# Optimization experiments

Measured on AMD Instinct MI355X. Metric: run time of the kernel, lower is better.

## Reference

```python
import jax, jax.numpy as jnp
import numpy as np

EPS = 1e-5
B, C, N_A, N_B, P, M = 128, 32, 12, 12, 8192, 2


def _bn(x, gamma, beta, mean, var):
    # x: (B, C, P); per-channel inference batch norm
    scale = gamma * jax.lax.rsqrt(var + EPS)
    return x * scale[None, :, None] + (beta - mean * scale)[None, :, None]


def setup_inputs() -> dict:
    key = jax.random.key(0)
    ks = jax.random.split(key, 12)
    return {
        "feat_a": jax.random.normal(ks[0], (B, C, N_A), jnp.float32),
        "feat_b": jax.random.normal(ks[1], (B, C, N_B), jnp.float32),
        "assign_a": jax.random.randint(ks[2], (P, M), 0, N_A, jnp.int32),
        "assign_b": jax.random.randint(ks[3], (P, M), 0, N_B, jnp.int32),
        "bn1_gamma": jax.random.uniform(ks[4], (C,), jnp.float32, 0.5, 1.5),
        "bn1_beta": jax.random.normal(ks[5], (C,), jnp.float32) * 0.1,
        "bn1_mean": jax.random.normal(ks[6], (C,), jnp.float32) * 0.1,
        "bn1_var": jax.random.uniform(ks[7], (C,), jnp.float32, 0.5, 1.5),
        "conv_w": jax.random.normal(ks[8], (C, C), jnp.float32) / np.sqrt(C),
        "bn2_gamma": jax.random.uniform(ks[9], (C,), jnp.float32, 0.5, 1.5),
        "bn2_beta": jax.random.normal(ks[10], (C,), jnp.float32) * 0.1,
        "bn2_mean": jax.random.normal(ks[11], (C,), jnp.float32) * 0.1,
        "bn2_var": jnp.ones((C,), jnp.float32),
    }


def reference(feat_a, feat_b, assign_a, assign_b,
              bn1_gamma, bn1_beta, bn1_mean, bn1_var,
              conv_w, bn2_gamma, bn2_beta, bn2_mean, bn2_var):
    # Gather product features via permutation indices: (B, C, P, M)
    ga = feat_a[:, :, assign_a].max(axis=-1)  # max over constituents -> (B, C, P)
    gb = feat_b[:, :, assign_b].max(axis=-1)
    agg = jnp.maximum(ga, gb)                 # 'max' aggregation across products
    x = _bn(agg, bn1_gamma, bn1_beta, bn1_mean, bn1_var)
    x = jnp.einsum('oc,bcp->bop', conv_w, x)  # 1x1 Conv1d, no bias
    x = _bn(x, bn2_gamma, bn2_beta, bn2_mean, bn2_var)
    return jax.nn.relu(x)
```

## Files before the change

kernel.cpp:

```cpp
#include <hip/hip_runtime.h>


#define EPS 1e-5f
constexpr int B   = 128;
constexpr int C   = 32;
constexpr int NA  = 12;
constexpr int PP  = 8192;
constexpr int PT  = 256;
constexpr int FS  = 36;
constexpr int XS  = 40;
constexpr int W2S = 36;

typedef short bfv8  __attribute__((ext_vector_type(8)));
typedef float f32x4 __attribute__((ext_vector_type(4)));

__device__ __forceinline__ ushort f2bf(float f) {
    uint u = __float_as_uint(f);
    u += 0x7fffu + ((u >> 16) & 1u);
    return (ushort)(u >> 16);
}
__device__ __forceinline__ float bf2f(ushort h) {
    return __uint_as_float(((uint)h) << 16);
}
__device__ __forceinline__ uint pk(ushort lo, ushort hi) {
    return (uint)lo | ((uint)hi << 16);
}

__global__ __launch_bounds__(256) void main_kernel(
    const float* __restrict__ feat_a, const float* __restrict__ feat_b,
    const int*   __restrict__ assign_a, const int* __restrict__ assign_b,
    const float* __restrict__ conv_w,
    const float* __restrict__ g1, const float* __restrict__ b1,
    const float* __restrict__ m1, const float* __restrict__ v1,
    const float* __restrict__ g2, const float* __restrict__ b2,
    const float* __restrict__ m2, const float* __restrict__ v2,
    float* __restrict__ out)
{
    __shared__ float s1[C], t1[C], s2v[C], bsh[C];
    __shared__ __align__(16) float  w2[C * W2S];
    __shared__ __align__(16) float  fa[NA * FS];
    __shared__ __align__(16) float  fb[NA * FS];
    __shared__ __align__(16) ushort xh[PT * XS];

    const int tid  = threadIdx.x;
    const int lane = tid & 63;
    const int b    = blockIdx.x >> 5;
    const int p0   = (blockIdx.x & 31) * PT;
    const int q    = lane >> 4;
    const int n    = lane & 15;

    if (tid < C) {
        float s = g1[tid] * rsqrtf(v1[tid] + EPS);
        s1[tid]  = s;
        t1[tid]  = b1[tid] - m1[tid] * s;
        s2v[tid] = g2[tid] * rsqrtf(v2[tid] + EPS);
    }
    for (int i = tid; i < C * NA; i += 256) {
        int c = i / NA, nn = i - c * NA;
        fa[nn * FS + c] = feat_a[b * C * NA + i];
        fb[nn * FS + c] = feat_b[b * C * NA + i];
    }
    __syncthreads();

    for (int i = tid; i < C * C; i += 256) {
        int o = i >> 5, c = i & 31;
        w2[o * W2S + c] = conv_w[i] * s1[c] * s2v[o];
    }
    if (tid < C) {
        float acc = 0.f;
        for (int c = 0; c < C; ++c) acc += conv_w[tid * C + c] * t1[c];
        bsh[tid] = acc * s2v[tid] + (b2[tid] - m2[tid] * s2v[tid]);
    }
    __syncthreads();

    bfv8 ah0, al0, ah1, al1;
    {
        float wv0[8], wv1[8];
        const float* r0 = &w2[(lane & 15) * W2S + q * 8];
        const float* r1 = &w2[((lane & 15) + 16) * W2S + q * 8];
        *(float4*)&wv0[0] = *(const float4*)(r0);
        *(float4*)&wv0[4] = *(const float4*)(r0 + 4);
        *(float4*)&wv1[0] = *(const float4*)(r1);
        *(float4*)&wv1[4] = *(const float4*)(r1 + 4);
#pragma unroll
        for (int j = 0; j < 8; ++j) {
            ushort h0 = f2bf(wv0[j]);
            ah0[j] = (short)h0;
            al0[j] = (short)f2bf(wv0[j] - bf2f(h0));
            ushort h1 = f2bf(wv1[j]);
            ah1[j] = (short)h1;
            al1[j] = (short)f2bf(wv1[j] - bf2f(h1));
        }
    }
    float bias0[4], bias1[4];
#pragma unroll
    for (int r = 0; r < 4; ++r) {
        bias0[r] = bsh[q * 4 + r];
        bias1[r] = bsh[16 + q * 4 + r];
    }

    {
        const int p = p0 + tid;
        const int2 ia = ((const int2*)assign_a)[p];
        const int2 ib = ((const int2*)assign_b)[p];
        const float* a0 = &fa[ia.x * FS];
        const float* a1 = &fa[ia.y * FS];
        const float* c0 = &fb[ib.x * FS];
        const float* c1 = &fb[ib.y * FS];

        float x[C];
#pragma unroll
        for (int cc = 0; cc < C; cc += 4) {
            float4 va0 = *(const float4*)(a0 + cc);
            float4 va1 = *(const float4*)(a1 + cc);
            float4 vb0 = *(const float4*)(c0 + cc);
            float4 vb1 = *(const float4*)(c1 + cc);
            x[cc + 0] = fmaxf(fmaxf(va0.x, va1.x), fmaxf(vb0.x, vb1.x));
            x[cc + 1] = fmaxf(fmaxf(va0.y, va1.y), fmaxf(vb0.y, vb1.y));
            x[cc + 2] = fmaxf(fmaxf(va0.z, va1.z), fmaxf(vb0.z, vb1.z));
            x[cc + 3] = fmaxf(fmaxf(va0.w, va1.w), fmaxf(vb0.w, vb1.w));
        }

        ushort* rowh = &xh[tid * XS];
        const int rot = (tid + (tid >> 3)) & 3;
#pragma unroll
        for (int g = 0; g < 4; ++g) {
            const int c = g * 8;
            ushort h[8];
#pragma unroll
            for (int j = 0; j < 8; ++j) h[j] = f2bf(x[c + j]);
            uint4 vh = make_uint4(pk(h[0], h[1]), pk(h[2], h[3]),
                                  pk(h[4], h[5]), pk(h[6], h[7]));
            *(uint4*)(rowh + ((g + rot) & 3) * 8) = vh;
        }
    }
    __syncthreads();

    const int wave = tid >> 6;
    const f32x4 zero = {0.f, 0.f, 0.f, 0.f};
    float* outb = out + b * C * PP + p0;
#pragma unroll
    for (int ch = 0; ch < 4; ++ch) {
        const int base = (wave * 4 + ch) * 16;
        const int r    = base + n;
        const int slot = (q + r + (r >> 3)) & 3;
        const bfv8 bh  = *(const bfv8*)&xh[r * XS + slot * 8];

        f32x4 d0 = __builtin_amdgcn_mfma_f32_16x16x32_bf16(ah0, bh, zero, 0, 0, 0);
        d0       = __builtin_amdgcn_mfma_f32_16x16x32_bf16(al0, bh, d0,   0, 0, 0);
        f32x4 d1 = __builtin_amdgcn_mfma_f32_16x16x32_bf16(ah1, bh, zero, 0, 0, 0);
        d1       = __builtin_amdgcn_mfma_f32_16x16x32_bf16(al1, bh, d1,   0, 0, 0);

        float* op = outb + base + n;
#pragma unroll
        for (int rr = 0; rr < 4; ++rr) {
            op[(q * 4 + rr) * PP]      = fmaxf(d0[rr] + bias0[rr], 0.f);
            op[(16 + q * 4 + rr) * PP] = fmaxf(d1[rr] + bias1[rr], 0.f);
        }
    }
}

extern "C" void kernel_launch(void* const* d_in, const int* in_sizes, int n_in,
                              void* d_out, int out_size, void* d_ws, size_t ws_size,
                              hipStream_t stream) {
    const float* feat_a   = (const float*)d_in[0];
    const float* feat_b   = (const float*)d_in[1];
    const int*   assign_a = (const int*)  d_in[2];
    const int*   assign_b = (const int*)  d_in[3];
    const float* g1 = (const float*)d_in[4];
    const float* b1 = (const float*)d_in[5];
    const float* m1 = (const float*)d_in[6];
    const float* v1 = (const float*)d_in[7];
    const float* cw = (const float*)d_in[8];
    const float* g2 = (const float*)d_in[9];
    const float* b2 = (const float*)d_in[10];
    const float* m2 = (const float*)d_in[11];
    const float* v2 = (const float*)d_in[12];

    float* out = (float*)d_out;
    (void)d_ws; (void)ws_size;

    main_kernel<<<B * (PP / PT), 256, 0, stream>>>(
        feat_a, feat_b, assign_a, assign_b, cw,
        g1, b1, m1, v1, g2, b2, m2, v2, out);
}
```

Before: 171.4 us.

## Switch gather and MFMA to fp16 with packed max and vectorized output stores

Stores the gathered features in LDS as fp16 and computes the max with v_pk_max_f16 on packed pairs. This replaces per-element fp32 max plus the bf16 conversion, and halves the LDS read traffic. The MFMA switches from bf16 to f16 with the operands swapped, so each lane holds 4 consecutive points of one output channel and can write them with float4 stores instead of scalar strided stores. The bias matvec becomes a wave shuffle reduction. Rounding the inputs to fp16 cuts their precision, and large feature values could overflow fp16.

```diff
diff --git a/kernel.cpp b/kernel.cpp
--- a/kernel.cpp
+++ b/kernel.cpp
@@ -7,23 +7,17 @@
 constexpr int NA  = 12;
 constexpr int PP  = 8192;
 constexpr int PT  = 256;
-constexpr int FS  = 36;
+constexpr int FS  = 40;
 constexpr int XS  = 40;
 constexpr int W2S = 36;
 
-typedef short bfv8  __attribute__((ext_vector_type(8)));
-typedef float f32x4 __attribute__((ext_vector_type(4)));
+typedef _Float16 f16x8 __attribute__((ext_vector_type(8)));
+typedef float    f32x4 __attribute__((ext_vector_type(4)));
 
-__device__ __forceinline__ ushort f2bf(float f) {
-    uint u = __float_as_uint(f);
-    u += 0x7fffu + ((u >> 16) & 1u);
-    return (ushort)(u >> 16);
-}
-__device__ __forceinline__ float bf2f(ushort h) {
-    return __uint_as_float(((uint)h) << 16);
-}
-__device__ __forceinline__ uint pk(ushort lo, ushort hi) {
-    return (uint)lo | ((uint)hi << 16);
+__device__ __forceinline__ uint pkmax(uint a, uint b) {
+    uint d;
+    asm("v_pk_max_f16 %0, %1, %2" : "=v"(d) : "v"(a), "v"(b));
+    return d;
 }
 
 __global__ __launch_bounds__(256) void main_kernel(
@@ -37,10 +31,10 @@
     float* __restrict__ out)
 {
     __shared__ float s1[C], t1[C], s2v[C], bsh[C];
-    __shared__ __align__(16) float  w2[C * W2S];
-    __shared__ __align__(16) float  fa[NA * FS];
-    __shared__ __align__(16) float  fb[NA * FS];
-    __shared__ __align__(16) ushort xh[PT * XS];
+    __shared__ __align__(16) float     w2[C * W2S];
+    __shared__ __align__(16) _Float16  fa[NA * FS];
+    __shared__ __align__(16) _Float16  fb[NA * FS];
+    __shared__ __align__(16) ushort    xh[PT * XS];
 
     const int tid  = threadIdx.x;
     const int lane = tid & 63;
@@ -57,81 +51,83 @@
     }
     for (int i = tid; i < C * NA; i += 256) {
         int c = i / NA, nn = i - c * NA;
-        fa[nn * FS + c] = feat_a[b * C * NA + i];
-        fb[nn * FS + c] = feat_b[b * C * NA + i];
+        fa[nn * FS + c] = (_Float16)feat_a[b * C * NA + i];
+        fb[nn * FS + c] = (_Float16)feat_b[b * C * NA + i];
     }
     __syncthreads();
 
-    for (int i = tid; i < C * C; i += 256) {
-        int o = i >> 5, c = i & 31;
-        w2[o * W2S + c] = conv_w[i] * s1[c] * s2v[o];
-    }
-    if (tid < C) {
-        float acc = 0.f;
-        for (int c = 0; c < C; ++c) acc += conv_w[tid * C + c] * t1[c];
-        bsh[tid] = acc * s2v[tid] + (b2[tid] - m2[tid] * s2v[tid]);
+    {
+        float bpart[4];
+#pragma unroll
+        for (int it = 0; it < 4; ++it) {
+            int i = tid + it * 256;
+            int o = i >> 5, c = i & 31;
+            float cw = conv_w[i];
+            w2[o * W2S + c] = cw * s1[c] * s2v[o];
+            bpart[it] = cw * t1[c];
+        }
+#pragma unroll
+        for (int m = 16; m >= 1; m >>= 1) {
+#pragma unroll
+            for (int it = 0; it < 4; ++it)
+                bpart[it] += __shfl_xor(bpart[it], m, 64);
+        }
+        if ((tid & 31) == 0) {
+            int o0 = tid >> 5;
+#pragma unroll
+            for (int it = 0; it < 4; ++it) {
+                int o = o0 + it * 8;
+                bsh[o] = bpart[it] * s2v[o] + (b2[o] - m2[o] * s2v[o]);
+            }
+        }
     }
     __syncthreads();
 
-    bfv8 ah0, al0, ah1, al1;
+    f16x8 wh0, wl0, wh1, wl1;
     {
         float wv0[8], wv1[8];
-        const float* r0 = &w2[(lane & 15) * W2S + q * 8];
-        const float* r1 = &w2[((lane & 15) + 16) * W2S + q * 8];
+        const float* r0 = &w2[n * W2S + q * 8];
+        const float* r1 = &w2[(n + 16) * W2S + q * 8];
         *(float4*)&wv0[0] = *(const float4*)(r0);
         *(float4*)&wv0[4] = *(const float4*)(r0 + 4);
         *(float4*)&wv1[0] = *(const float4*)(r1);
         *(float4*)&wv1[4] = *(const float4*)(r1 + 4);
 #pragma unroll
         for (int j = 0; j < 8; ++j) {
-            ushort h0 = f2bf(wv0[j]);
-            ah0[j] = (short)h0;
-            al0[j] = (short)f2bf(wv0[j] - bf2f(h0));
-            ushort h1 = f2bf(wv1[j]);
-            ah1[j] = (short)h1;
-            al1[j] = (short)f2bf(wv1[j] - bf2f(h1));
+            _Float16 h0 = (_Float16)wv0[j];
+            wh0[j] = h0;
+            wl0[j] = (_Float16)(wv0[j] - (float)h0);
+            _Float16 h1 = (_Float16)wv1[j];
+            wh1[j] = h1;
+            wl1[j] = (_Float16)(wv1[j] - (float)h1);
         }
     }
-    float bias0[4], bias1[4];
-#pragma unroll
-    for (int r = 0; r < 4; ++r) {
-        bias0[r] = bsh[q * 4 + r];
-        bias1[r] = bsh[16 + q * 4 + r];
-    }
+    const float bias_lo = bsh[n];
+    const float bias_hi = bsh[16 + n];
 
     {
         const int p = p0 + tid;
         const int2 ia = ((const int2*)assign_a)[p];
         const int2 ib = ((const int2*)assign_b)[p];
-        const float* a0 = &fa[ia.x * FS];
-        const float* a1 = &fa[ia.y * FS];
-        const float* c0 = &fb[ib.x * FS];
-        const float* c1 = &fb[ib.y * FS];
-
-        float x[C];
-#pragma unroll
-        for (int cc = 0; cc < C; cc += 4) {
-            float4 va0 = *(const float4*)(a0 + cc);
-            float4 va1 = *(const float4*)(a1 + cc);
-            float4 vb0 = *(const float4*)(c0 + cc);
-            float4 vb1 = *(const float4*)(c1 + cc);
-            x[cc + 0] = fmaxf(fmaxf(va0.x, va1.x), fmaxf(vb0.x, vb1.x));
-            x[cc + 1] = fmaxf(fmaxf(va0.y, va1.y), fmaxf(vb0.y, vb1.y));
-            x[cc + 2] = fmaxf(fmaxf(va0.z, va1.z), fmaxf(vb0.z, vb1.z));
-            x[cc + 3] = fmaxf(fmaxf(va0.w, va1.w), fmaxf(vb0.w, vb1.w));
-        }
+        const _Float16* a0 = &fa[ia.x * FS];
+        const _Float16* a1 = &fa[ia.y * FS];
+        const _Float16* c0 = &fb[ib.x * FS];
+        const _Float16* c1 = &fb[ib.y * FS];
 
         ushort* rowh = &xh[tid * XS];
         const int rot = (tid + (tid >> 3)) & 3;
 #pragma unroll
         for (int g = 0; g < 4; ++g) {
-            const int c = g * 8;
-            ushort h[8];
-#pragma unroll
-            for (int j = 0; j < 8; ++j) h[j] = f2bf(x[c + j]);
-            uint4 vh = make_uint4(pk(h[0], h[1]), pk(h[2], h[3]),
-                                  pk(h[4], h[5]), pk(h[6], h[7]));
-            *(uint4*)(rowh + ((g + rot) & 3) * 8) = vh;
+            uint4 va0 = *(const uint4*)(a0 + g * 8);
+            uint4 va1 = *(const uint4*)(a1 + g * 8);
+            uint4 vb0 = *(const uint4*)(c0 + g * 8);
+            uint4 vb1 = *(const uint4*)(c1 + g * 8);
+            uint4 m;
+            m.x = pkmax(pkmax(va0.x, va1.x), pkmax(vb0.x, vb1.x));
+            m.y = pkmax(pkmax(va0.y, va1.y), pkmax(vb0.y, vb1.y));
+            m.z = pkmax(pkmax(va0.z, va1.z), pkmax(vb0.z, vb1.z));
+            m.w = pkmax(pkmax(va0.w, va1.w), pkmax(vb0.w, vb1.w));
+            *(uint4*)(rowh + ((g + rot) & 3) * 8) = m;
         }
     }
     __syncthreads();
@@ -144,19 +140,25 @@
         const int base = (wave * 4 + ch) * 16;
         const int r    = base + n;
         const int slot = (q + r + (r >> 3)) & 3;
-        const bfv8 bh  = *(const bfv8*)&xh[r * XS + slot * 8];
+        const f16x8 xa = *(const f16x8*)&xh[r * XS + slot * 8];
 
-        f32x4 d0 = __builtin_amdgcn_mfma_f32_16x16x32_bf16(ah0, bh, zero, 0, 0, 0);
-        d0       = __builtin_amdgcn_mfma_f32_16x16x32_bf16(al0, bh, d0,   0, 0, 0);
-        f32x4 d1 = __builtin_amdgcn_mfma_f32_16x16x32_bf16(ah1, bh, zero, 0, 0, 0);
-        d1       = __builtin_amdgcn_mfma_f32_16x16x32_bf16(al1, bh, d1,   0, 0, 0);
+        f32x4 d0 = __builtin_amdgcn_mfma_f32_16x16x32_f16(xa, wh0, zero, 0, 0, 0);
+        d0       = __builtin_amdgcn_mfma_f32_16x16x32_f16(xa, wl0, d0,   0, 0, 0);
+        f32x4 d1 = __builtin_amdgcn_mfma_f32_16x16x32_f16(xa, wh1, zero, 0, 0, 0);
+        d1       = __builtin_amdgcn_mfma_f32_16x16x32_f16(xa, wl1, d1,   0, 0, 0);
 
-        float* op = outb + base + n;
-#pragma unroll
-        for (int rr = 0; rr < 4; ++rr) {
-            op[(q * 4 + rr) * PP]      = fmaxf(d0[rr] + bias0[rr], 0.f);
-            op[(16 + q * 4 + rr) * PP] = fmaxf(d1[rr] + bias1[rr], 0.f);
-        }
+        float* op = outb + base + q * 4;
+        float4 v0, v1;
+        v0.x = fmaxf(d0[0] + bias_lo, 0.f);
+        v0.y = fmaxf(d0[1] + bias_lo, 0.f);
+        v0.z = fmaxf(d0[2] + bias_lo, 0.f);
+        v0.w = fmaxf(d0[3] + bias_lo, 0.f);
+        v1.x = fmaxf(d1[0] + bias_hi, 0.f);
+        v1.y = fmaxf(d1[1] + bias_hi, 0.f);
+        v1.z = fmaxf(d1[2] + bias_hi, 0.f);
+        v1.w = fmaxf(d1[3] + bias_hi, 0.f);
+        *(float4*)(op + n * PP)        = v0;
+        *(float4*)(op + (16 + n) * PP) = v1;
     }
 }
 
```

Result: no change. 170.2 us (-0.7%).
